# Performance work log

Hardware: AMD Instinct MI355X
Metric: run time of the kernel (lower is better)

The kernel has to match this reference:

```python
import jax, jax.numpy as jnp
import numpy as np

B, T, HID = 2, 2048, 4096
H, KV, D = 32, 4, 128
GROUP = H // KV
SCALE = D ** -0.5
EPS = 1e-6
ROPE_BASE = 10000.0


def rope(x, dims=D, base=ROPE_BASE):
    # mlx-style non-traditional RoPE (rotate halves). x: [B, h, T, D]
    t = x.shape[2]
    inv_freq = base ** (-jnp.arange(0, dims, 2, dtype=jnp.float32) / dims)  # [D/2]
    theta = jnp.arange(t, dtype=jnp.float32)[:, None] * inv_freq[None, :]   # [T, D/2]
    cos, sin = jnp.cos(theta), jnp.sin(theta)
    x1, x2 = x[..., : dims // 2], x[..., dims // 2 :]
    return jnp.concatenate([x1 * cos - x2 * sin, x1 * sin + x2 * cos], axis=-1).astype(x.dtype)


def setup_inputs() -> dict:
    key = jax.random.key(0)
    k1, k2, k3 = jax.random.split(key, 3)
    hidden_states = jax.random.normal(k1, (B, T, HID), dtype=jnp.float32)
    Wqkv = jax.random.normal(k2, ((H + 2 * KV) * D, HID), dtype=jnp.float32) * 0.02
    Wo = jax.random.normal(k3, (HID, H * D), dtype=jnp.float32) * 0.02
    q_weight = jnp.ones((H, D), dtype=jnp.float32)
    k_weight = jnp.ones((KV, D), dtype=jnp.float32)
    return {"hidden_states": hidden_states, "Wqkv": Wqkv, "Wo": Wo,
            "q_weight": q_weight, "k_weight": k_weight}


def reference(hidden_states, Wqkv, Wo, q_weight, k_weight):
    x = hidden_states
    qkv = jnp.einsum('btc,oc->bto', x, Wqkv)
    q, k, v = jnp.split(qkv, [H * D, H * D + KV * D], axis=-1)
    q = q.reshape(B, T, H, D).transpose(0, 2, 1, 3)    # [B,H,T,D]
    k = k.reshape(B, T, KV, D).transpose(0, 2, 1, 3)   # [B,KV,T,D]
    v = v.reshape(B, T, KV, D).transpose(0, 2, 1, 3)
    # Faithful to source: q/k are REPLACED by rsqrt(mean(q^2)) * weight (no q multiply)
    q = jax.lax.rsqrt(jnp.mean(q * q, axis=-1, keepdims=True) + EPS) * q_weight[:, None, :]
    k = jax.lax.rsqrt(jnp.mean(k * k, axis=-1, keepdims=True) + EPS) * k_weight[:, None, :]
    q = rope(q)
    k = rope(k)
    # GQA: repeat kv heads
    k = jnp.repeat(k, GROUP, axis=1)  # [B,H,T,D]
    v = jnp.repeat(v, GROUP, axis=1)
    scores = jnp.einsum('bhqd,bhkd->bhqk', q, k) * SCALE
    attn = jax.nn.softmax(scores, axis=-1)
    out = jnp.einsum('bhqk,bhkd->bhqd', attn, v)
    out = out.transpose(0, 2, 1, 3).reshape(B, T, H * D)
    return jnp.einsum('bto,co->btc', out, Wo)
```

## Files before the change

kernel.cpp:

```cpp
#include <hip/hip_runtime.h>

typedef __bf16 bf16_t;
typedef __bf16 bf16x4 __attribute__((ext_vector_type(4)));
typedef __bf16 bf16x8 __attribute__((ext_vector_type(8)));
typedef float floatx4 __attribute__((ext_vector_type(4)));

__device__ __forceinline__ float bf2f(bf16_t x) { return (float)x; }
__device__ __forceinline__ bf16_t f2bf(float x) { return (bf16_t)x; }

__device__ __forceinline__ void async_copy16(const bf16_t* g, bf16_t* l) {
    __builtin_amdgcn_global_load_lds(
        (const __attribute__((address_space(1))) unsigned int*)g,
        (__attribute__((address_space(3))) unsigned int*)l, 16, 0, 0);
}

__global__ __launch_bounds__(256) void cvt_f32_bf16(const float* __restrict__ in,
                                                    bf16_t* __restrict__ out,
                                                    int n8) {
    int i = blockIdx.x * blockDim.x + threadIdx.x;
    if (i >= n8) return;
    const float4* p = (const float4*)in + (size_t)i * 2;
    float4 a = p[0], b = p[1];
    bf16x8 v;
    v[0] = f2bf(a.x); v[1] = f2bf(a.y); v[2] = f2bf(a.z); v[3] = f2bf(a.w);
    v[4] = f2bf(b.x); v[5] = f2bf(b.y); v[6] = f2bf(b.z); v[7] = f2bf(b.w);
    *(bf16x8*)(out + (size_t)i * 8) = v;
}

template <typename OT>
__global__ __launch_bounds__(256) void gemm_bt(const bf16_t* __restrict__ A,
                                               const bf16_t* __restrict__ B,
                                               OT* __restrict__ C,
                                               int M, int N, int K) {
    __shared__ __attribute__((aligned(16))) bf16_t As[128 * 32];
    __shared__ __attribute__((aligned(16))) bf16_t Bs[128 * 32];
    const int tid = threadIdx.x;
    const int lane = tid & 63;
    const int w = tid >> 6;
    const int l15 = lane & 15, qd = lane >> 4;
    const int tm = blockIdx.y * 128, tn = blockIdx.x * 128;
    const int wm = (w >> 1) * 64, wn = (w & 1) * 64;

    floatx4 acc[4][4] = {};

    for (int k0 = 0; k0 < K; k0 += 32) {
#pragma unroll
        for (int it = 0; it < 2; ++it) {
            int c = it * 256 + tid;
            int row = c >> 2, col = (c & 3) * 8;
            async_copy16(&A[(size_t)(tm + row) * K + k0 + col], &As[c * 8]);
            async_copy16(&B[(size_t)(tn + row) * K + k0 + col], &Bs[c * 8]);
        }
        __syncthreads();
        bf16x8 af[4], bfr[4];
#pragma unroll
        for (int i = 0; i < 4; i++)
            af[i] = *(const bf16x8*)&As[(wm + i * 16 + l15) * 32 + qd * 8];
#pragma unroll
        for (int j = 0; j < 4; j++)
            bfr[j] = *(const bf16x8*)&Bs[(wn + j * 16 + l15) * 32 + qd * 8];
#pragma unroll
        for (int i = 0; i < 4; i++)
#pragma unroll
            for (int j = 0; j < 4; j++)
                acc[i][j] = __builtin_amdgcn_mfma_f32_16x16x32_bf16(
                    af[i], bfr[j], acc[i][j], 0, 0, 0);
        __syncthreads();
    }
#pragma unroll
    for (int i = 0; i < 4; i++) {
        int row = tm + wm + i * 16 + qd * 4;
#pragma unroll
        for (int j = 0; j < 4; j++) {
            int col = tn + wn + j * 16 + l15;
#pragma unroll
            for (int r = 0; r < 4; r++)
                C[(size_t)(row + r) * N + col] = (OT)acc[i][j][r];
        }
    }
}

__global__ __launch_bounds__(256) void rmsrope(const bf16_t* __restrict__ qkv,
                                               const float* __restrict__ qw,
                                               const float* __restrict__ kw,
                                               bf16_t* __restrict__ q_r,
                                               bf16_t* __restrict__ k_r,
                                               bf16_t* __restrict__ v_r) {
    const int tid = threadIdx.x, lane = tid & 63, w = tid >> 6;
    const int slot = blockIdx.x * 4 + w;
    const int row = slot / 40;
    const int hs = slot - row * 40;
    const int b = row >> 11, t = row & 2047;
    const bf16_t* src = qkv + (size_t)row * 5120 + hs * 128;

    if (hs >= 36) {
        size_t dst = ((size_t)((b * 4 + (hs - 36)) * 2048 + t)) * 128;
        v_r[dst + lane] = src[lane];
        v_r[dst + lane + 64] = src[lane + 64];
        return;
    }
    float x1 = bf2f(src[lane]);
    float x2 = bf2f(src[lane + 64]);
    float ss = x1 * x1 + x2 * x2;
#pragma unroll
    for (int off = 1; off < 64; off <<= 1) ss += __shfl_xor(ss, off);
    const float rr = rsqrtf(ss * (1.0f / 128.0f) + 1e-6f);

    const float* wp;
    bf16_t* dstp;
    if (hs < 32) {
        wp = qw + hs * 128;
        dstp = q_r + ((size_t)((b * 32 + hs) * 2048 + t)) * 128;
    } else {
        wp = kw + (hs - 32) * 128;
        dstp = k_r + ((size_t)((b * 4 + (hs - 32)) * 2048 + t)) * 128;
    }
    float n1 = rr * wp[lane];
    float n2 = rr * wp[lane + 64];
    float inv_freq = exp2f((float)lane * -0.20762050593046f);
    float th = (float)t * inv_freq;
    float sn, cs;
    sincosf(th, &sn, &cs);
    dstp[lane] = f2bf(n1 * cs - n2 * sn);
    dstp[lane + 64] = f2bf(n1 * sn + n2 * cs);
}

#define ATT_SCALE 0.08838834764831845f

__global__ __launch_bounds__(256, 2) void flash_attn(const bf16_t* __restrict__ Qr,
                                                     const bf16_t* __restrict__ Kr,
                                                     const bf16_t* __restrict__ Vr,
                                                     bf16_t* __restrict__ Oo) {
    __shared__ __attribute__((aligned(16))) bf16_t Ks[64 * 136];
    __shared__ __attribute__((aligned(16))) bf16_t Vts[128 * 72];
    __shared__ __attribute__((aligned(16))) bf16_t Ps[4][32 * 72];
    const int tid = threadIdx.x, lane = tid & 63, w = tid >> 6;
    const int l15 = lane & 15, qd = lane >> 4;
    const int qt = blockIdx.x, bh = blockIdx.y;
    const int b = bh >> 5, h = bh & 31;
    const int kvh = h >> 3;
    const bf16_t* Qb = Qr + ((size_t)(b * 32 + h) * 2048 + qt * 128) * 128;
    const bf16_t* Kb = Kr + ((size_t)(b * 4 + kvh) * 2048) * 128;
    const bf16_t* Vb = Vr + ((size_t)(b * 4 + kvh) * 2048) * 128;
    const int wrow = w * 32;
    const int pi = l15 * 4 + qd;

    bf16x8 qf[2][4];
#pragma unroll
    for (int i = 0; i < 2; i++)
#pragma unroll
        for (int kk = 0; kk < 4; kk++)
            qf[i][kk] = *(const bf16x8*)&Qb[(size_t)(wrow + i * 16 + l15) * 128 +
                                            kk * 32 + qd * 8];

    float m_s[2][4], l_s[2][4];
    floatx4 oacc[2][8] = {};
#pragma unroll
    for (int i = 0; i < 2; i++)
#pragma unroll
        for (int r = 0; r < 4; r++) { m_s[i][r] = -1e30f; l_s[i][r] = 0.0f; }

    for (int kt = 0; kt < 32; ++kt) {
        __syncthreads();
#pragma unroll
        for (int it = 0; it < 4; ++it) {
            int c = it * 256 + tid;
            int row = c >> 4, col = (c & 15) * 8;
            *(bf16x8*)&Ks[row * 136 + col] =
                *(const bf16x8*)&Kb[(size_t)(kt * 64 + row) * 128 + col];
        }
#pragma unroll
        for (int it = 0; it < 4; ++it) {
            int d0 = (it * 4 + w) * 8;
            bf16x8 v = *(const bf16x8*)&Vb[(size_t)(kt * 64 + lane) * 128 + d0];
#pragma unroll
            for (int e = 0; e < 8; ++e) Vts[(d0 + e) * 72 + pi] = v[e];
        }
        __syncthreads();

        floatx4 sacc[2][4] = {};
#pragma unroll
        for (int kk = 0; kk < 4; kk++) {
            bf16x8 bfr[4];
#pragma unroll
            for (int j = 0; j < 4; j++)
                bfr[j] = *(const bf16x8*)&Ks[(j * 16 + l15) * 136 + kk * 32 + qd * 8];
#pragma unroll
            for (int i = 0; i < 2; i++)
#pragma unroll
                for (int j = 0; j < 4; j++)
                    sacc[i][j] = __builtin_amdgcn_mfma_f32_16x16x32_bf16(
                        qf[i][kk], bfr[j], sacc[i][j], 0, 0, 0);
        }

#pragma unroll
        for (int i = 0; i < 2; i++) {
#pragma unroll
            for (int r = 0; r < 4; r++) {
                float s0 = sacc[i][0][r] * ATT_SCALE;
                float s1 = sacc[i][1][r] * ATT_SCALE;
                float s2 = sacc[i][2][r] * ATT_SCALE;
                float s3 = sacc[i][3][r] * ATT_SCALE;
                float mx = fmaxf(fmaxf(s0, s1), fmaxf(s2, s3));
#pragma unroll
                for (int off = 1; off < 16; off <<= 1)
                    mx = fmaxf(mx, __shfl_xor(mx, off));
                float mnew = fmaxf(m_s[i][r], mx);
                float alpha = __expf(m_s[i][r] - mnew);
                float p0 = __expf(s0 - mnew), p1 = __expf(s1 - mnew);
                float p2 = __expf(s2 - mnew), p3 = __expf(s3 - mnew);
                float rs = (p0 + p1) + (p2 + p3);
#pragma unroll
                for (int off = 1; off < 16; off <<= 1) rs += __shfl_xor(rs, off);
                l_s[i][r] = l_s[i][r] * alpha + rs;
                m_s[i][r] = mnew;
                bf16x4 pv;
                pv[0] = f2bf(p0); pv[1] = f2bf(p1);
                pv[2] = f2bf(p2); pv[3] = f2bf(p3);
                *(bf16x4*)&Ps[w][(i * 16 + qd * 4 + r) * 72 + l15 * 4] = pv;
#pragma unroll
                for (int jo = 0; jo < 8; jo++) oacc[i][jo][r] *= alpha;
            }
        }

#pragma unroll
        for (int kk = 0; kk < 64; kk += 32) {
            bf16x8 pf[2], vf[8];
#pragma unroll
            for (int i = 0; i < 2; i++)
                pf[i] = *(const bf16x8*)&Ps[w][(i * 16 + l15) * 72 + kk + qd * 8];
#pragma unroll
            for (int jo = 0; jo < 8; jo++)
                vf[jo] = *(const bf16x8*)&Vts[(jo * 16 + l15) * 72 + kk + qd * 8];
#pragma unroll
            for (int i = 0; i < 2; i++)
#pragma unroll
                for (int jo = 0; jo < 8; jo++)
                    oacc[i][jo] = __builtin_amdgcn_mfma_f32_16x16x32_bf16(
                        pf[i], vf[jo], oacc[i][jo], 0, 0, 0);
        }
    }

#pragma unroll
    for (int i = 0; i < 2; i++) {
#pragma unroll
        for (int r = 0; r < 4; r++) {
            float inv = 1.0f / l_s[i][r];
            int tg = qt * 128 + wrow + i * 16 + qd * 4 + r;
            size_t base = ((size_t)b * 2048 + tg) * 4096 + h * 128;
#pragma unroll
            for (int jo = 0; jo < 8; jo++)
                Oo[base + jo * 16 + l15] = f2bf(oacc[i][jo][r] * inv);
        }
    }
}

extern "C" void kernel_launch(void* const* d_in, const int* in_sizes, int n_in,
                              void* d_out, int out_size, void* d_ws, size_t ws_size,
                              hipStream_t stream) {
    const float* hidden = (const float*)d_in[0];
    const float* Wqkv   = (const float*)d_in[1];
    const float* Wo     = (const float*)d_in[2];
    const float* qw     = (const float*)d_in[3];
    const float* kw     = (const float*)d_in[4];
    float* out = (float*)d_out;

    char* ws = (char*)d_ws;
    bf16_t* Wqkv_bf   = (bf16_t*)ws;
    bf16_t* q_r       = (bf16_t*)ws;
    bf16_t* k_r       = (bf16_t*)(ws + 33554432ull);
    bf16_t* v_r       = (bf16_t*)(ws + 37748736ull);
    bf16_t* hidden_bf = (bf16_t*)(ws + 41943040ull);
    bf16_t* attn      = (bf16_t*)(ws + 41943040ull);
    bf16_t* qkv       = (bf16_t*)(ws + 75497472ull);
    bf16_t* Wo_bf     = (bf16_t*)(ws + 75497472ull);

    hipLaunchKernelGGL(cvt_f32_bf16, dim3(8192), dim3(256), 0, stream,
                       hidden, hidden_bf, 16777216 / 8);
    hipLaunchKernelGGL(cvt_f32_bf16, dim3(10240), dim3(256), 0, stream,
                       Wqkv, Wqkv_bf, 20971520 / 8);
    hipLaunchKernelGGL((gemm_bt<bf16_t>), dim3(40, 32), dim3(256), 0, stream,
                       hidden_bf, Wqkv_bf, qkv, 4096, 5120, 4096);
    hipLaunchKernelGGL(rmsrope, dim3(40960), dim3(256), 0, stream,
                       qkv, qw, kw, q_r, k_r, v_r);
    hipLaunchKernelGGL(cvt_f32_bf16, dim3(8192), dim3(256), 0, stream,
                       Wo, Wo_bf, 16777216 / 8);
    hipLaunchKernelGGL(flash_attn, dim3(16, 64), dim3(256), 0, stream,
                       q_r, k_r, v_r, attn);
    hipLaunchKernelGGL((gemm_bt<float>), dim3(32, 32), dim3(256), 0, stream,
                       attn, Wo_bf, out, 4096, 4096, 4096);
}
```

Measured before the change: 1.008 ms.

## Fold softmax scale into Q, lazy rescale, MFMA row sums, swizzled async K loads

The softmax scale and log2(e) are folded into Q during the norm/RoPE pass, so the attention loop uses exp2f directly on the raw scores. The running max is only updated, and O rescaled, when some lane's tile max exceeds the stored max by a threshold; this is checked with a wave-wide vote. Row sums now come from an extra MFMA of P against a ones vector instead of shuffle reductions. K tiles are loaded into an XOR-swizzled, unpadded LDS layout with global_load_lds async copies. Together these cut VALU, shuffle and exp work in the inner loop. The trade-off is that stale maxima allow exponents up to about 2^11.5, which can lose accuracy in bf16 P, and Q now carries an extra bf16 rounding of the scale.

```diff
diff --git a/kernel.cpp b/kernel.cpp
--- a/kernel.cpp
+++ b/kernel.cpp
@@ -108,15 +108,18 @@
 
     const float* wp;
     bf16_t* dstp;
+    float sc;
     if (hs < 32) {
         wp = qw + hs * 128;
         dstp = q_r + ((size_t)((b * 32 + hs) * 2048 + t)) * 128;
+        sc = rr * (0.08838834764831845f * 1.4426950408889634f);
     } else {
         wp = kw + (hs - 32) * 128;
         dstp = k_r + ((size_t)((b * 4 + (hs - 32)) * 2048 + t)) * 128;
-    }
-    float n1 = rr * wp[lane];
-    float n2 = rr * wp[lane + 64];
+        sc = rr;
+    }
+    float n1 = sc * wp[lane];
+    float n2 = sc * wp[lane + 64];
     float inv_freq = exp2f((float)lane * -0.20762050593046f);
     float th = (float)t * inv_freq;
     float sn, cs;
@@ -125,13 +128,11 @@
     dstp[lane + 64] = f2bf(n1 * sn + n2 * cs);
 }
 
-#define ATT_SCALE 0.08838834764831845f
-
 __global__ __launch_bounds__(256, 2) void flash_attn(const bf16_t* __restrict__ Qr,
                                                      const bf16_t* __restrict__ Kr,
                                                      const bf16_t* __restrict__ Vr,
                                                      bf16_t* __restrict__ Oo) {
-    __shared__ __attribute__((aligned(16))) bf16_t Ks[64 * 136];
+    __shared__ __attribute__((aligned(16))) bf16_t Ks[64 * 128];
     __shared__ __attribute__((aligned(16))) bf16_t Vts[128 * 72];
     __shared__ __attribute__((aligned(16))) bf16_t Ps[4][32 * 72];
     const int tid = threadIdx.x, lane = tid & 63, w = tid >> 6;
@@ -153,21 +154,27 @@
             qf[i][kk] = *(const bf16x8*)&Qb[(size_t)(wrow + i * 16 + l15) * 128 +
                                             kk * 32 + qd * 8];
 
-    float m_s[2][4], l_s[2][4];
+    bf16x8 onef;
+#pragma unroll
+    for (int e = 0; e < 8; ++e) onef[e] = f2bf(1.0f);
+
+    float m_s[2][4];
+    floatx4 lacc[2] = {};
     floatx4 oacc[2][8] = {};
 #pragma unroll
     for (int i = 0; i < 2; i++)
 #pragma unroll
-        for (int r = 0; r < 4; r++) { m_s[i][r] = -1e30f; l_s[i][r] = 0.0f; }
+        for (int r = 0; r < 4; r++) m_s[i][r] = -1e30f;
 
     for (int kt = 0; kt < 32; ++kt) {
         __syncthreads();
 #pragma unroll
         for (int it = 0; it < 4; ++it) {
-            int c = it * 256 + tid;
-            int row = c >> 4, col = (c & 15) * 8;
-            *(bf16x8*)&Ks[row * 136 + col] =
-                *(const bf16x8*)&Kb[(size_t)(kt * 64 + row) * 128 + col];
+            int cc = it * 256 + tid;
+            int row = cc >> 4;
+            int xb = ((cc & 15) * 16) ^ ((row & 7) << 4);
+            async_copy16(&Kb[(size_t)(kt * 64 + row) * 128 + (xb >> 1)],
+                         &Ks[cc * 8]);
         }
 #pragma unroll
         for (int it = 0; it < 4; ++it) {
@@ -183,8 +190,11 @@
         for (int kk = 0; kk < 4; kk++) {
             bf16x8 bfr[4];
 #pragma unroll
-            for (int j = 0; j < 4; j++)
-                bfr[j] = *(const bf16x8*)&Ks[(j * 16 + l15) * 136 + kk * 32 + qd * 8];
+            for (int j = 0; j < 4; j++) {
+                int rr2 = j * 16 + l15;
+                int xb = (kk * 64 + qd * 16) ^ ((rr2 & 7) << 4);
+                bfr[j] = *(const bf16x8*)&Ks[rr2 * 128 + (xb >> 1)];
+            }
 #pragma unroll
             for (int i = 0; i < 2; i++)
 #pragma unroll
@@ -193,35 +203,45 @@
                         qf[i][kk], bfr[j], sacc[i][j], 0, 0, 0);
         }
 
-#pragma unroll
-        for (int i = 0; i < 2; i++) {
+        float mxv[2][4];
+        int fneed = 0;
+#pragma unroll
+        for (int i = 0; i < 2; i++)
 #pragma unroll
             for (int r = 0; r < 4; r++) {
-                float s0 = sacc[i][0][r] * ATT_SCALE;
-                float s1 = sacc[i][1][r] * ATT_SCALE;
-                float s2 = sacc[i][2][r] * ATT_SCALE;
-                float s3 = sacc[i][3][r] * ATT_SCALE;
-                float mx = fmaxf(fmaxf(s0, s1), fmaxf(s2, s3));
+                float mx = fmaxf(fmaxf(sacc[i][0][r], sacc[i][1][r]),
+                                 fmaxf(sacc[i][2][r], sacc[i][3][r]));
 #pragma unroll
                 for (int off = 1; off < 16; off <<= 1)
                     mx = fmaxf(mx, __shfl_xor(mx, off));
-                float mnew = fmaxf(m_s[i][r], mx);
-                float alpha = __expf(m_s[i][r] - mnew);
-                float p0 = __expf(s0 - mnew), p1 = __expf(s1 - mnew);
-                float p2 = __expf(s2 - mnew), p3 = __expf(s3 - mnew);
-                float rs = (p0 + p1) + (p2 + p3);
-#pragma unroll
-                for (int off = 1; off < 16; off <<= 1) rs += __shfl_xor(rs, off);
-                l_s[i][r] = l_s[i][r] * alpha + rs;
-                m_s[i][r] = mnew;
+                mxv[i][r] = mx;
+                fneed |= (mx > m_s[i][r] + 11.5f);
+            }
+        if (__any(fneed)) {
+#pragma unroll
+            for (int i = 0; i < 2; i++)
+#pragma unroll
+                for (int r = 0; r < 4; r++) {
+                    float mnew = fmaxf(m_s[i][r], mxv[i][r]);
+                    float alpha = exp2f(m_s[i][r] - mnew);
+                    m_s[i][r] = mnew;
+#pragma unroll
+                    for (int jo = 0; jo < 8; jo++) oacc[i][jo][r] *= alpha;
+                    lacc[i][r] *= alpha;
+                }
+        }
+#pragma unroll
+        for (int i = 0; i < 2; i++)
+#pragma unroll
+            for (int r = 0; r < 4; r++) {
+                float m = m_s[i][r];
                 bf16x4 pv;
-                pv[0] = f2bf(p0); pv[1] = f2bf(p1);
-                pv[2] = f2bf(p2); pv[3] = f2bf(p3);
+                pv[0] = f2bf(exp2f(sacc[i][0][r] - m));
+                pv[1] = f2bf(exp2f(sacc[i][1][r] - m));
+                pv[2] = f2bf(exp2f(sacc[i][2][r] - m));
+                pv[3] = f2bf(exp2f(sacc[i][3][r] - m));
                 *(bf16x4*)&Ps[w][(i * 16 + qd * 4 + r) * 72 + l15 * 4] = pv;
-#pragma unroll
-                for (int jo = 0; jo < 8; jo++) oacc[i][jo][r] *= alpha;
             }
-        }
 
 #pragma unroll
         for (int kk = 0; kk < 64; kk += 32) {
@@ -233,11 +253,14 @@
             for (int jo = 0; jo < 8; jo++)
                 vf[jo] = *(const bf16x8*)&Vts[(jo * 16 + l15) * 72 + kk + qd * 8];
 #pragma unroll
-            for (int i = 0; i < 2; i++)
+            for (int i = 0; i < 2; i++) {
+                lacc[i] = __builtin_amdgcn_mfma_f32_16x16x32_bf16(
+                    pf[i], onef, lacc[i], 0, 0, 0);
 #pragma unroll
                 for (int jo = 0; jo < 8; jo++)
                     oacc[i][jo] = __builtin_amdgcn_mfma_f32_16x16x32_bf16(
                         pf[i], vf[jo], oacc[i][jo], 0, 0, 0);
+            }
         }
     }
 
@@ -245,7 +268,7 @@
     for (int i = 0; i < 2; i++) {
 #pragma unroll
         for (int r = 0; r < 4; r++) {
-            float inv = 1.0f / l_s[i][r];
+            float inv = 1.0f / lacc[i][r];
             int tg = qt * 128 + wrow + i * 16 + qd * 4 + r;
             size_t base = ((size_t)b * 2048 + tg) * 4096 + h * 128;
 #pragma unroll
```

Result: faster. 957.7 us (-5.0%).
